# Kernel optimization log

Measured on AMD Instinct MI355X. Metric: run time of the kernel, lower is better.

Reference implementation:

```python
import jax, jax.numpy as jnp
import numpy as np

N, E, F_IN, F_OUT, E_DIM = 8192, 65536, 256, 64, 32


def _xavier(k, shape, gain):
    fan_out, fan_in = shape
    bound = gain * jnp.sqrt(6.0 / (fan_in + fan_out))
    return jax.random.uniform(k, shape, jnp.float32, -bound, bound)


def setup_inputs() -> dict:
    key = jax.random.key(0)
    ks = jax.random.split(key, 10)
    gain = float(np.sqrt(2.0))  # calculate_gain('relu')
    return {
        "h_neigh": jax.random.normal(ks[0], (N, F_IN), jnp.float32),
        "h_self": jax.random.normal(ks[1], (N, F_IN), jnp.float32),
        "edge_features": jax.random.normal(ks[2], (E, E_DIM), jnp.float32),
        "W_preagg": _xavier(ks[3], (F_OUT, F_IN), gain),
        "W_self": _xavier(ks[4], (F_OUT, F_OUT), gain),
        "W_neigh": _xavier(ks[5], (F_OUT, F_OUT), gain),
        "W_edge": _xavier(ks[6], (F_OUT * F_OUT, E_DIM), gain),
        "b_edge": jnp.zeros((F_OUT * F_OUT,), jnp.float32),
        "src": jax.random.randint(ks[7], (E,), 0, N, jnp.int32),
        "dst": jax.random.randint(ks[8], (E,), 0, N, jnp.int32),
    }


def reference(h_neigh, h_self, edge_features, W_preagg, W_self, W_neigh, W_edge, b_edge, src, dst):
    relu = jax.nn.relu
    # fc_preagg (Linear no-bias + ReLU); dropout p=0 -> identity (eval mode)
    hn = relu(h_neigh @ W_preagg.T)   # [N, F_OUT]
    hs = relu(h_self @ W_preagg.T)    # [N, F_OUT]
    # edge_fc: Linear(edge_dim, F*F) + ReLU, viewed as [E, F, F]
    ew = relu(edge_features @ W_edge.T + b_edge).reshape(E, F_OUT, F_OUT)
    # DGL u_mul_e broadcast: m[e,i,j] = hn[src[e], j] * ew[e,i,j]
    # then mean over in-edges per dst node, then sum over dim i.
    # mean/sum commute with the i-sum, so fold i first: s[e,j] = sum_i ew[e,i,j]
    s = ew.sum(axis=1)                # [E, F_OUT]
    msg = hn[src] * s                 # [E, F_OUT]
    agg = jax.ops.segment_sum(msg, dst, num_segments=N)                      # [N, F_OUT]
    deg = jax.ops.segment_sum(jnp.ones((E,), jnp.float32), dst, num_segments=N)
    neigh = agg / jnp.maximum(deg, 1.0)[:, None]  # mean (0 for isolated nodes, as DGL)
    # fc_self / fc_neigh each include a ReLU, plus the outer ReLU
    z = relu(relu(hs @ W_self.T) + relu(neigh @ W_neigh.T))
    return z
```

## Files before the change

kernel.cpp:

```cpp
#include <hip/hip_runtime.h>
#include <hip/hip_bf16.h>

typedef __attribute__((ext_vector_type(8))) short bf16x8;
typedef __attribute__((ext_vector_type(4))) float f32x4;
typedef __attribute__((ext_vector_type(4))) unsigned int u32x4;

#define NNODES 8192
#define NEDGES 65536
#define FIN 256
#define FOUT 64
#define EDIM 32

#define WS_HN    0x000000u
#define WS_HS    0x200000u
#define WS_MSG   0x400000u
#define WS_DEG   0x1400000u
#define WS_OFF   0x1408000u
#define WS_RANK  0x1410000u
#define WS_PERM  0x1450000u
#define WS_GSRC  0x1490000u
#define WS_WBF   0x14D0000u
#define WS_WPRET 0x1510000u
#define WS_WST   0x1520000u
#define WS_WNT   0x1524000u

__device__ __forceinline__ unsigned short f2bf(float f) {
    unsigned u = __builtin_bit_cast(unsigned, f);
    u = (u + 0x7fffu + ((u >> 16) & 1u)) >> 16;
    return (unsigned short)u;
}

__global__ void prep_kernel(const float* __restrict__ W_edge,
                            const float* __restrict__ W_preagg,
                            const float* __restrict__ W_self,
                            const float* __restrict__ W_neigh,
                            unsigned short* __restrict__ wbf,
                            float* __restrict__ wpreT,
                            float* __restrict__ wsT,
                            float* __restrict__ wnT) {
    int i = blockIdx.x * 256 + threadIdx.x;
    if (i < FOUT * FOUT * EDIM) wbf[i] = f2bf(W_edge[i]);
    if (i < FOUT * FIN) {
        int o = i >> 8, k = i & 255;
        wpreT[k * FOUT + o] = W_preagg[i];
    }
    if (i < FOUT * FOUT) {
        int o = i >> 6, k = i & 63;
        wsT[k * FOUT + o] = W_self[i];
        wnT[k * FOUT + o] = W_neigh[i];
    }
}

__global__ void count_kernel(const int* __restrict__ dst,
                             int* __restrict__ deg,
                             int* __restrict__ rank) {
    int e = blockIdx.x * 256 + threadIdx.x;
    rank[e] = atomicAdd(deg + dst[e], 1);
}

__global__ __launch_bounds__(256) void scan_kernel(const int* __restrict__ deg,
                                                   int* __restrict__ off) {
    __shared__ int wsum[4];
    int t = threadIdx.x, lane = t & 63, w = t >> 6;
    int base = t * 32;
    int loc[32];
    int s = 0;
    #pragma unroll
    for (int i = 0; i < 32; ++i) { loc[i] = s; s += deg[base + i]; }
    int v = s;
    #pragma unroll
    for (int d = 1; d < 64; d <<= 1) {
        int u = __shfl_up(v, d);
        if (lane >= d) v += u;
    }
    if (lane == 63) wsum[w] = v;
    int threadExcl = v - s;
    __syncthreads();
    int wexcl = 0;
    for (int i = 0; i < w; ++i) wexcl += wsum[i];
    int tbase = wexcl + threadExcl;
    #pragma unroll
    for (int i = 0; i < 32; ++i) off[base + i] = tbase + loc[i];
}

__global__ void fill_kernel(const int* __restrict__ src,
                            const int* __restrict__ dst,
                            const int* __restrict__ off,
                            const int* __restrict__ rank,
                            int* __restrict__ perm,
                            int* __restrict__ gsrc) {
    int e = blockIdx.x * 256 + threadIdx.x;
    int slot = off[dst[e]] + rank[e];
    perm[slot] = e;
    gsrc[slot] = src[e];
}

__global__ __launch_bounds__(256) void preagg_kernel(const float* __restrict__ h_neigh,
                                                     const float* __restrict__ h_self,
                                                     const float* __restrict__ wpreT,
                                                     float* __restrict__ hn,
                                                     float* __restrict__ hs) {
    __shared__ float hrow[32 * FIN];
    const float* srcp = blockIdx.y ? h_self : h_neigh;
    float* outp = blockIdx.y ? hs : hn;
    int t = threadIdx.x;
    size_t row0 = (size_t)blockIdx.x * 32;
    {
        const float4* g = reinterpret_cast<const float4*>(srcp + row0 * FIN);
        float4* l = reinterpret_cast<float4*>(hrow);
        #pragma unroll
        for (int it = 0; it < 8; ++it)
            l[t + 256 * it] = g[t + 256 * it];
    }
    __syncthreads();
    int o = t & 63, wr = t >> 6;
    float acc[8] = {0.f, 0.f, 0.f, 0.f, 0.f, 0.f, 0.f, 0.f};
    for (int k4 = 0; k4 < FIN; k4 += 4) {
        float w0 = wpreT[(k4 + 0) * FOUT + o];
        float w1 = wpreT[(k4 + 1) * FOUT + o];
        float w2 = wpreT[(k4 + 2) * FOUT + o];
        float w3 = wpreT[(k4 + 3) * FOUT + o];
        #pragma unroll
        for (int rr = 0; rr < 8; ++rr) {
            float4 h4 = *reinterpret_cast<const float4*>(&hrow[(wr * 8 + rr) * FIN + k4]);
            acc[rr] = fmaf(h4.x, w0, acc[rr]);
            acc[rr] = fmaf(h4.y, w1, acc[rr]);
            acc[rr] = fmaf(h4.z, w2, acc[rr]);
            acc[rr] = fmaf(h4.w, w3, acc[rr]);
        }
    }
    #pragma unroll
    for (int rr = 0; rr < 8; ++rr)
        outp[(row0 + wr * 8 + rr) * FOUT + o] = fmaxf(acc[rr], 0.f);
}

__global__ __launch_bounds__(512, 4) void edge_gemm_kernel(
    const float* __restrict__ ef,
    const unsigned short* __restrict__ wbf,
    const float* __restrict__ b_edge,
    float* __restrict__ msg) {
    __shared__ __align__(16) unsigned short bsm[16384];
    int tid = threadIdx.x;
    int wave = tid >> 6, lane = tid & 63;
    int rowm = lane & 15, kc = lane >> 4, k0 = kc * 8;
    int mw = wave >> 2, cw = wave & 3;
    int e0 = blockIdx.x * 128 + mw * 64;

    bf16x8 a[4];
    #pragma unroll
    for (int t = 0; t < 4; ++t) {
        const float* p = ef + (size_t)(e0 + t * 16 + rowm) * EDIM + k0;
        float4 v0 = reinterpret_cast<const float4*>(p)[0];
        float4 v1 = reinterpret_cast<const float4*>(p)[1];
        bf16x8 aa;
        aa[0] = (short)f2bf(v0.x); aa[1] = (short)f2bf(v0.y);
        aa[2] = (short)f2bf(v0.z); aa[3] = (short)f2bf(v0.w);
        aa[4] = (short)f2bf(v1.x); aa[5] = (short)f2bf(v1.y);
        aa[6] = (short)f2bf(v1.z); aa[7] = (short)f2bf(v1.w);
        a[t] = aa;
    }

    f32x4 sacc[4];
    #pragma unroll
    for (int t = 0; t < 4; ++t) sacc[t] = f32x4{0.f, 0.f, 0.f, 0.f};
    const f32x4 z4 = {0.f, 0.f, 0.f, 0.f};

    for (int s = 0; s < 8; ++s) {
        __syncthreads();
        {
            const u32x4* g = reinterpret_cast<const u32x4*>(wbf) + s * 2048;
            u32x4* l = reinterpret_cast<u32x4*>(bsm);
            #pragma unroll
            for (int it = 0; it < 4; ++it)
                l[tid + 512 * it] = g[tid + 512 * it];
        }
        __syncthreads();
        const float* bias_p = b_edge + s * 512 + cw * 16 + rowm;
        #pragma unroll
        for (int il = 0; il < 8; ++il) {
            int col_local = il * 64 + cw * 16 + rowm;
            bf16x8 b = *reinterpret_cast<const bf16x8*>(
                reinterpret_cast<const char*>(bsm) + col_local * 64 + kc * 16);
            float bias = bias_p[il * 64];
            f32x4 cin = {bias, bias, bias, bias};
            #pragma unroll
            for (int t = 0; t < 4; ++t) {
                f32x4 d = __builtin_amdgcn_mfma_f32_16x16x32_bf16(a[t], b, cin, 0, 0, 0);
                sacc[t] += __builtin_elementwise_max(d, z4);
            }
        }
    }

    #pragma unroll
    for (int t = 0; t < 4; ++t) {
        #pragma unroll
        for (int r = 0; r < 4; ++r) {
            size_t e = (size_t)(e0 + t * 16 + kc * 4 + r);
            msg[e * FOUT + cw * 16 + rowm] = sacc[t][r];
        }
    }
}

__global__ __launch_bounds__(256) void final_kernel(
    const float* __restrict__ hs,
    const float* __restrict__ hn,
    const float* __restrict__ msg,
    const int* __restrict__ deg,
    const int* __restrict__ off,
    const int* __restrict__ perm,
    const int* __restrict__ gsrc,
    const float* __restrict__ wsT,
    const float* __restrict__ wnT,
    float* __restrict__ out) {
    __shared__ float sm[4][2][FOUT];
    int t = threadIdx.x, w = t >> 6, lane = t & 63;
    int n = blockIdx.x * 4 + w;
    int o0 = off[n], d = deg[n];
    float acc = 0.f;
    int i = 0;
    for (; i + 2 <= d; i += 2) {
        int ea = perm[o0 + i], sa = gsrc[o0 + i];
        int eb = perm[o0 + i + 1], sb = gsrc[o0 + i + 1];
        float ma = msg[(size_t)ea * FOUT + lane];
        float ha = hn[(size_t)sa * FOUT + lane];
        float mb = msg[(size_t)eb * FOUT + lane];
        float hb = hn[(size_t)sb * FOUT + lane];
        acc = fmaf(ma, ha, acc);
        acc = fmaf(mb, hb, acc);
    }
    if (i < d) {
        int ea = perm[o0 + i], sa = gsrc[o0 + i];
        acc = fmaf(msg[(size_t)ea * FOUT + lane], hn[(size_t)sa * FOUT + lane], acc);
    }
    float neigh = acc / fmaxf((float)d, 1.f);
    sm[w][0][lane] = neigh;
    sm[w][1][lane] = hs[(size_t)n * FOUT + lane];
    __syncthreads();
    float a1 = 0.f, a2 = 0.f;
    #pragma unroll 8
    for (int k = 0; k < FOUT; ++k) {
        a1 = fmaf(sm[w][1][k], wsT[k * FOUT + lane], a1);
        a2 = fmaf(sm[w][0][k], wnT[k * FOUT + lane], a2);
    }
    out[(size_t)n * FOUT + lane] = fmaxf(fmaxf(a1, 0.f) + fmaxf(a2, 0.f), 0.f);
}

extern "C" void kernel_launch(void* const* d_in, const int* in_sizes, int n_in,
                              void* d_out, int out_size, void* d_ws, size_t ws_size,
                              hipStream_t stream) {
    const float* h_neigh  = (const float*)d_in[0];
    const float* h_self   = (const float*)d_in[1];
    const float* ef       = (const float*)d_in[2];
    const float* W_preagg = (const float*)d_in[3];
    const float* W_self   = (const float*)d_in[4];
    const float* W_neigh  = (const float*)d_in[5];
    const float* W_edge   = (const float*)d_in[6];
    const float* b_edge   = (const float*)d_in[7];
    const int*   src      = (const int*)d_in[8];
    const int*   dst      = (const int*)d_in[9];
    float* out = (float*)d_out;
    char* ws = (char*)d_ws;

    float* hn    = (float*)(ws + WS_HN);
    float* hs    = (float*)(ws + WS_HS);
    float* msg   = (float*)(ws + WS_MSG);
    int*   deg   = (int*)(ws + WS_DEG);
    int*   off   = (int*)(ws + WS_OFF);
    int*   rank  = (int*)(ws + WS_RANK);
    int*   perm  = (int*)(ws + WS_PERM);
    int*   gsrc  = (int*)(ws + WS_GSRC);
    unsigned short* wbf = (unsigned short*)(ws + WS_WBF);
    float* wpreT = (float*)(ws + WS_WPRET);
    float* wsT   = (float*)(ws + WS_WST);
    float* wnT   = (float*)(ws + WS_WNT);

    hipMemsetAsync(ws + WS_DEG, 0, 0x8000, stream);

    prep_kernel<<<512, 256, 0, stream>>>(W_edge, W_preagg, W_self, W_neigh,
                                         wbf, wpreT, wsT, wnT);
    count_kernel<<<NEDGES / 256, 256, 0, stream>>>(dst, deg, rank);
    scan_kernel<<<1, 256, 0, stream>>>(deg, off);
    fill_kernel<<<NEDGES / 256, 256, 0, stream>>>(src, dst, off, rank, perm, gsrc);
    preagg_kernel<<<dim3(256, 2), 256, 0, stream>>>(h_neigh, h_self, wpreT, hn, hs);
    edge_gemm_kernel<<<512, 512, 0, stream>>>(ef, wbf, b_edge, msg);
    final_kernel<<<NNODES / 4, 256, 0, stream>>>(hs, hn, msg, deg, off, perm, gsrc,
                                                 wsT, wnT, out);
}
```

Measured before the change: 100.6 us.

## Merge independent launches into block-specialized kernels and stream edge weights from global

Independent stages are merged into shared launches using block-index specialization: prep with count, preagg with scan, and edge GEMM with fill. This cuts the launch count from seven to four and lets independent work run side by side. The edge GEMM no longer stages W_edge through LDS with barriers; each lane instead loads its bf16 B fragments directly from global/L2 with a one-group register prefetch. The trade-off is more global/L2 traffic per block and heterogeneous blocks sharing one launch configuration.

Result: faster. 84.57 us (-16.0%).

```diff
diff --git a/kernel.cpp b/kernel.cpp
--- a/kernel.cpp
+++ b/kernel.cpp
@@ -3,7 +3,6 @@
 
 typedef __attribute__((ext_vector_type(8))) short bf16x8;
 typedef __attribute__((ext_vector_type(4))) float f32x4;
-typedef __attribute__((ext_vector_type(4))) unsigned int u32x4;
 
 #define NNODES 8192
 #define NEDGES 65536
@@ -30,81 +29,74 @@
     return (unsigned short)u;
 }
 
-__global__ void prep_kernel(const float* __restrict__ W_edge,
-                            const float* __restrict__ W_preagg,
-                            const float* __restrict__ W_self,
-                            const float* __restrict__ W_neigh,
-                            unsigned short* __restrict__ wbf,
-                            float* __restrict__ wpreT,
-                            float* __restrict__ wsT,
-                            float* __restrict__ wnT) {
-    int i = blockIdx.x * 256 + threadIdx.x;
-    if (i < FOUT * FOUT * EDIM) wbf[i] = f2bf(W_edge[i]);
-    if (i < FOUT * FIN) {
-        int o = i >> 8, k = i & 255;
-        wpreT[k * FOUT + o] = W_preagg[i];
-    }
-    if (i < FOUT * FOUT) {
-        int o = i >> 6, k = i & 63;
-        wsT[k * FOUT + o] = W_self[i];
-        wnT[k * FOUT + o] = W_neigh[i];
-    }
-}
-
-__global__ void count_kernel(const int* __restrict__ dst,
-                             int* __restrict__ deg,
-                             int* __restrict__ rank) {
-    int e = blockIdx.x * 256 + threadIdx.x;
-    rank[e] = atomicAdd(deg + dst[e], 1);
-}
-
-__global__ __launch_bounds__(256) void scan_kernel(const int* __restrict__ deg,
-                                                   int* __restrict__ off) {
+__global__ __launch_bounds__(256) void prep_count_kernel(
+    const float* __restrict__ W_edge,
+    const float* __restrict__ W_preagg,
+    const float* __restrict__ W_self,
+    const float* __restrict__ W_neigh,
+    const int* __restrict__ dst,
+    unsigned short* __restrict__ wbf,
+    float* __restrict__ wpreT,
+    float* __restrict__ wsT,
+    float* __restrict__ wnT,
+    int* __restrict__ deg,
+    int* __restrict__ rank) {
+    int b = blockIdx.x, t = threadIdx.x;
+    if (b < 512) {
+        int i = b * 256 + t;
+        if (i < FOUT * FOUT * EDIM) wbf[i] = f2bf(W_edge[i]);
+        if (i < FOUT * FIN) {
+            int o = i >> 8, k = i & 255;
+            wpreT[k * FOUT + o] = W_preagg[i];
+        }
+        if (i < FOUT * FOUT) {
+            int o = i >> 6, k = i & 63;
+            wsT[k * FOUT + o] = W_self[i];
+            wnT[k * FOUT + o] = W_neigh[i];
+        }
+    } else {
+        int e = (b - 512) * 256 + t;
+        rank[e] = atomicAdd(deg + dst[e], 1);
+    }
+}
+
+__global__ __launch_bounds__(256) void preagg_scan_kernel(
+    const float* __restrict__ h_neigh,
+    const float* __restrict__ h_self,
+    const float* __restrict__ wpreT,
+    const int* __restrict__ deg,
+    float* __restrict__ hn,
+    float* __restrict__ hs,
+    int* __restrict__ off) {
+    __shared__ float hrow[32 * FIN];
     __shared__ int wsum[4];
-    int t = threadIdx.x, lane = t & 63, w = t >> 6;
-    int base = t * 32;
-    int loc[32];
-    int s = 0;
-    #pragma unroll
-    for (int i = 0; i < 32; ++i) { loc[i] = s; s += deg[base + i]; }
-    int v = s;
-    #pragma unroll
-    for (int d = 1; d < 64; d <<= 1) {
-        int u = __shfl_up(v, d);
-        if (lane >= d) v += u;
-    }
-    if (lane == 63) wsum[w] = v;
-    int threadExcl = v - s;
-    __syncthreads();
-    int wexcl = 0;
-    for (int i = 0; i < w; ++i) wexcl += wsum[i];
-    int tbase = wexcl + threadExcl;
-    #pragma unroll
-    for (int i = 0; i < 32; ++i) off[base + i] = tbase + loc[i];
-}
-
-__global__ void fill_kernel(const int* __restrict__ src,
-                            const int* __restrict__ dst,
-                            const int* __restrict__ off,
-                            const int* __restrict__ rank,
-                            int* __restrict__ perm,
-                            int* __restrict__ gsrc) {
-    int e = blockIdx.x * 256 + threadIdx.x;
-    int slot = off[dst[e]] + rank[e];
-    perm[slot] = e;
-    gsrc[slot] = src[e];
-}
-
-__global__ __launch_bounds__(256) void preagg_kernel(const float* __restrict__ h_neigh,
-                                                     const float* __restrict__ h_self,
-                                                     const float* __restrict__ wpreT,
-                                                     float* __restrict__ hn,
-                                                     float* __restrict__ hs) {
-    __shared__ float hrow[32 * FIN];
-    const float* srcp = blockIdx.y ? h_self : h_neigh;
-    float* outp = blockIdx.y ? hs : hn;
-    int t = threadIdx.x;
-    size_t row0 = (size_t)blockIdx.x * 32;
+    int b = blockIdx.x, t = threadIdx.x;
+    if (b == 512) {
+        int lane = t & 63, w = t >> 6;
+        int base = t * 32;
+        int loc[32];
+        int s = 0;
+        #pragma unroll
+        for (int i = 0; i < 32; ++i) { loc[i] = s; s += deg[base + i]; }
+        int v = s;
+        #pragma unroll
+        for (int d = 1; d < 64; d <<= 1) {
+            int u = __shfl_up(v, d);
+            if (lane >= d) v += u;
+        }
+        if (lane == 63) wsum[w] = v;
+        int threadExcl = v - s;
+        __syncthreads();
+        int wexcl = 0;
+        for (int i = 0; i < w; ++i) wexcl += wsum[i];
+        int tbase = wexcl + threadExcl;
+        #pragma unroll
+        for (int i = 0; i < 32; ++i) off[base + i] = tbase + loc[i];
+        return;
+    }
+    const float* srcp = (b >> 8) ? h_self : h_neigh;
+    float* outp = (b >> 8) ? hs : hn;
+    size_t row0 = (size_t)(b & 255) * 32;
     {
         const float4* g = reinterpret_cast<const float4*>(srcp + row0 * FIN);
         float4* l = reinterpret_cast<float4*>(hrow);
@@ -134,17 +126,30 @@
         outp[(row0 + wr * 8 + rr) * FOUT + o] = fmaxf(acc[rr], 0.f);
 }
 
-__global__ __launch_bounds__(512, 4) void edge_gemm_kernel(
+__global__ __launch_bounds__(512, 4) void edge_fill_kernel(
     const float* __restrict__ ef,
     const unsigned short* __restrict__ wbf,
     const float* __restrict__ b_edge,
-    float* __restrict__ msg) {
-    __shared__ __align__(16) unsigned short bsm[16384];
-    int tid = threadIdx.x;
+    const int* __restrict__ src,
+    const int* __restrict__ dst,
+    const int* __restrict__ off,
+    const int* __restrict__ rank,
+    float* __restrict__ msg,
+    int* __restrict__ perm,
+    int* __restrict__ gsrc) {
+    int b = blockIdx.x, tid = threadIdx.x;
+    if (b >= 512) {
+        int e = (b - 512) * 512 + tid;
+        int slot = off[dst[e]] + rank[e];
+        perm[slot] = e;
+        gsrc[slot] = src[e];
+        return;
+    }
     int wave = tid >> 6, lane = tid & 63;
     int rowm = lane & 15, kc = lane >> 4, k0 = kc * 8;
     int mw = wave >> 2, cw = wave & 3;
-    int e0 = blockIdx.x * 128 + mw * 64;
+    int e0 = b * 128 + mw * 64;
+    int colbase = cw * 16 + rowm;
 
     bf16x8 a[4];
     #pragma unroll
@@ -164,28 +169,32 @@
     #pragma unroll
     for (int t = 0; t < 4; ++t) sacc[t] = f32x4{0.f, 0.f, 0.f, 0.f};
     const f32x4 z4 = {0.f, 0.f, 0.f, 0.f};
-
-    for (int s = 0; s < 8; ++s) {
-        __syncthreads();
-        {
-            const u32x4* g = reinterpret_cast<const u32x4*>(wbf) + s * 2048;
-            u32x4* l = reinterpret_cast<u32x4*>(bsm);
-            #pragma unroll
-            for (int it = 0; it < 4; ++it)
-                l[tid + 512 * it] = g[tid + 512 * it];
-        }
-        __syncthreads();
-        const float* bias_p = b_edge + s * 512 + cw * 16 + rowm;
-        #pragma unroll
-        for (int il = 0; il < 8; ++il) {
-            int col_local = il * 64 + cw * 16 + rowm;
-            bf16x8 b = *reinterpret_cast<const bf16x8*>(
-                reinterpret_cast<const char*>(bsm) + col_local * 64 + kc * 16);
-            float bias = bias_p[il * 64];
+    const char* wb = reinterpret_cast<const char*>(wbf);
+
+    bf16x8 bb[4];
+    float bs[4];
+    #pragma unroll
+    for (int p = 0; p < 4; ++p) {
+        bb[p] = *reinterpret_cast<const bf16x8*>(
+            wb + ((size_t)(p * 64 + colbase) * 64 + kc * 16));
+        bs[p] = b_edge[p * 64 + colbase];
+    }
+    #pragma unroll
+    for (int gb = 0; gb < 64; gb += 4) {
+        #pragma unroll
+        for (int p = 0; p < 4; ++p) {
+            bf16x8 bcur = bb[p];
+            float bias = bs[p];
+            int gn = gb + 4 + p;
+            if (gn < 64) {
+                bb[p] = *reinterpret_cast<const bf16x8*>(
+                    wb + ((size_t)(gn * 64 + colbase) * 64 + kc * 16));
+                bs[p] = b_edge[gn * 64 + colbase];
+            }
             f32x4 cin = {bias, bias, bias, bias};
             #pragma unroll
             for (int t = 0; t < 4; ++t) {
-                f32x4 d = __builtin_amdgcn_mfma_f32_16x16x32_bf16(a[t], b, cin, 0, 0, 0);
+                f32x4 d = __builtin_amdgcn_mfma_f32_16x16x32_bf16(a[t], bcur, cin, 0, 0, 0);
                 sacc[t] += __builtin_elementwise_max(d, z4);
             }
         }
@@ -276,13 +285,12 @@
 
     hipMemsetAsync(ws + WS_DEG, 0, 0x8000, stream);
 
-    prep_kernel<<<512, 256, 0, stream>>>(W_edge, W_preagg, W_self, W_neigh,
-                                         wbf, wpreT, wsT, wnT);
-    count_kernel<<<NEDGES / 256, 256, 0, stream>>>(dst, deg, rank);
-    scan_kernel<<<1, 256, 0, stream>>>(deg, off);
-    fill_kernel<<<NEDGES / 256, 256, 0, stream>>>(src, dst, off, rank, perm, gsrc);
-    preagg_kernel<<<dim3(256, 2), 256, 0, stream>>>(h_neigh, h_self, wpreT, hn, hs);
-    edge_gemm_kernel<<<512, 512, 0, stream>>>(ef, wbf, b_edge, msg);
+    prep_count_kernel<<<768, 256, 0, stream>>>(W_edge, W_preagg, W_self, W_neigh,
+                                               dst, wbf, wpreT, wsT, wnT, deg, rank);
+    preagg_scan_kernel<<<513, 256, 0, stream>>>(h_neigh, h_self, wpreT, deg,
+                                                hn, hs, off);
+    edge_fill_kernel<<<640, 512, 0, stream>>>(ef, wbf, b_edge, src, dst, off, rank,
+                                              msg, perm, gsrc);
     final_kernel<<<NNODES / 4, 256, 0, stream>>>(hs, hn, msg, deg, off, perm, gsrc,
                                                  wsT, wnT, out);
 }
```
